# Kernel tuning notes

Hardware: AMD Instinct MI355X
Metric: run time of the kernel (lower is better)

Reference implementation:

```python
import jax, jax.numpy as jnp
import numpy as np

N_NODES = 50000
IN_F = 512
OUT_F = 512
N_EDGES = 1600000
DROP_P = 0.5
NEG_SLOPE = 0.01  # torch LeakyReLU default


def leaky_relu(x):
    return jnp.where(x >= 0, x, NEG_SLOPE * x)


def setup_inputs() -> dict:
    key = jax.random.key(0)
    k1, k2, k3, k4, k5, k6 = jax.random.split(key, 6)
    x = jax.random.normal(k1, (N_NODES, IN_F), dtype=jnp.float32)
    W = jax.random.normal(k2, (OUT_F, IN_F), dtype=jnp.float32) * (1.0 / np.sqrt(IN_F))
    # inverted dropout mask: bernoulli(keep)/keep, keep = 1 - p
    keep = 1.0 - DROP_P
    drop_mask = (jax.random.uniform(k3, (N_NODES, IN_F)) < keep).astype(jnp.float32) / keep
    adj_vals = jax.random.uniform(k4, (N_EDGES,), dtype=jnp.float32)
    adj_rows = jax.random.randint(k5, (N_EDGES,), 0, N_NODES, dtype=jnp.int32)
    adj_cols = jax.random.randint(k6, (N_EDGES,), 0, N_NODES, dtype=jnp.int32)
    return {"x": x, "W": W, "drop_mask": drop_mask, "adj_vals": adj_vals,
            "adj_rows": adj_rows, "adj_cols": adj_cols}


def reference(x, W, drop_mask, adj_vals, adj_rows, adj_cols):
    # support = Linear(dropout(x)); Linear weight is [out, in] (torch convention)
    support = jnp.einsum('ni,oi->no', x * drop_mask, W)  # [N, out]
    h = leaky_relu(support)
    # sparse adj @ h: out[r] += v * h[c]
    msgs = adj_vals[:, None] * h[adj_cols]               # [E, out]
    agg = jax.ops.segment_sum(msgs, adj_rows, num_segments=N_NODES)
    return leaky_relu(agg)
```

## Files before the change

kernel.cpp:

```cpp
#include <hip/hip_runtime.h>

#define NROWS 50000
#define NFEAT 512
#define NEDGE 1600000
#define SLOPE 0.01f

typedef unsigned short u16;
typedef __attribute__((ext_vector_type(8))) short short8;
typedef __attribute__((ext_vector_type(4))) float f32x4;
typedef __attribute__((ext_vector_type(4))) int i32x4;
typedef __attribute__((ext_vector_type(2))) unsigned uintx2;
typedef __attribute__((ext_vector_type(8))) unsigned short u16x8;

__device__ __forceinline__ u16 f2bf(float f) {
  unsigned u = __float_as_uint(f);
  u += 0x7fffu + ((u >> 16) & 1u);
  return (u16)(u >> 16);
}
__device__ __forceinline__ float lrelu(float v) { return v >= 0.f ? v : SLOPE * v; }

__device__ __forceinline__ void gload_lds16(const u16* g, u16* l) {
  __builtin_amdgcn_global_load_lds((const __attribute__((address_space(1))) void*)g,
                                   (__attribute__((address_space(3))) void*)l, 16, 0, 0);
}

__global__ void prep_kernel(const float* __restrict__ x, const float* __restrict__ m,
                            u16* __restrict__ xd, const float* __restrict__ w,
                            u16* __restrict__ wb, const int* __restrict__ rows,
                            int* __restrict__ counts) {
  const int stride = gridDim.x * blockDim.x;
  const int tid0 = blockIdx.x * blockDim.x + threadIdx.x;
  for (int i = tid0; i < (NROWS * NFEAT) / 8; i += stride) {
    size_t b = (size_t)i * 2;
    f32x4 a0 = __builtin_nontemporal_load(&((const f32x4*)x)[b]);
    f32x4 a1 = __builtin_nontemporal_load(&((const f32x4*)x)[b + 1]);
    f32x4 m0 = __builtin_nontemporal_load(&((const f32x4*)m)[b]);
    f32x4 m1 = __builtin_nontemporal_load(&((const f32x4*)m)[b + 1]);
    u16x8 o;
    o[0] = f2bf(a0[0] * m0[0]); o[1] = f2bf(a0[1] * m0[1]);
    o[2] = f2bf(a0[2] * m0[2]); o[3] = f2bf(a0[3] * m0[3]);
    o[4] = f2bf(a1[0] * m1[0]); o[5] = f2bf(a1[1] * m1[1]);
    o[6] = f2bf(a1[2] * m1[2]); o[7] = f2bf(a1[3] * m1[3]);
    *(u16x8*)(xd + (size_t)i * 8) = o;
  }
  for (int i = tid0; i < (NFEAT * NFEAT) / 8; i += stride) {
    size_t b = (size_t)i * 2;
    f32x4 a0 = __builtin_nontemporal_load(&((const f32x4*)w)[b]);
    f32x4 a1 = __builtin_nontemporal_load(&((const f32x4*)w)[b + 1]);
    u16x8 o;
    o[0] = f2bf(a0[0]); o[1] = f2bf(a0[1]); o[2] = f2bf(a0[2]); o[3] = f2bf(a0[3]);
    o[4] = f2bf(a1[0]); o[5] = f2bf(a1[1]); o[6] = f2bf(a1[2]); o[7] = f2bf(a1[3]);
    *(u16x8*)(wb + (size_t)i * 8) = o;
  }
  for (int i = tid0; i < NEDGE / 4; i += stride) {
    i32x4 r4 = __builtin_nontemporal_load(&((const i32x4*)rows)[i]);
    atomicAdd(&counts[r4[0]], 1);
    atomicAdd(&counts[r4[1]], 1);
    atomicAdd(&counts[r4[2]], 1);
    atomicAdd(&counts[r4[3]], 1);
  }
}

__global__ void scan_kernel(const int* __restrict__ counts, int* __restrict__ offs) {
  __shared__ int wpre[17];
  const int t = threadIdx.x;
  const int lane = t & 63, w = t >> 6;
  const int beg = t * 64;
  i32x4 c4[16];
  int s = 0;
  if (beg < NROWS) {
#pragma unroll
    for (int g = 0; g < 16; ++g) {
      int idx = beg + g * 4;
      if (idx < NROWS) {
        c4[g] = ((const i32x4*)counts)[idx >> 2];
        s += c4[g][0] + c4[g][1] + c4[g][2] + c4[g][3];
      }
    }
  }
  int inc = s;
#pragma unroll
  for (int d = 1; d < 64; d <<= 1) {
    int u = __shfl_up(inc, d);
    if (lane >= d) inc += u;
  }
  if (lane == 63) wpre[w + 1] = inc;
  __syncthreads();
  if (t == 0) {
    wpre[0] = 0;
    for (int i = 1; i <= 16; ++i) wpre[i] += wpre[i - 1];
    offs[NROWS] = wpre[16];
  }
  __syncthreads();
  int run = wpre[w] + inc - s;
  if (beg < NROWS) {
#pragma unroll
    for (int g = 0; g < 16; ++g) {
      int idx = beg + g * 4;
      if (idx < NROWS) {
        i32x4 o;
        o[0] = run; run += c4[g][0];
        o[1] = run; run += c4[g][1];
        o[2] = run; run += c4[g][2];
        o[3] = run; run += c4[g][3];
        ((i32x4*)offs)[idx >> 2] = o;
      }
    }
  }
}

__global__ void scatter_kernel(const float* __restrict__ vals, const int* __restrict__ rows,
                               const int* __restrict__ cols, const int* __restrict__ offs,
                               int* __restrict__ cursor, unsigned* __restrict__ svc) {
  int e0 = (blockIdx.x * blockDim.x + threadIdx.x) * 4;
  if (e0 >= NEDGE) return;
  i32x4 r4 = __builtin_nontemporal_load((const i32x4*)(rows + e0));
  i32x4 c4 = __builtin_nontemporal_load((const i32x4*)(cols + e0));
  f32x4 v4 = __builtin_nontemporal_load((const f32x4*)(vals + e0));
#pragma unroll
  for (int j = 0; j < 4; ++j) {
    int p = offs[r4[j]] + atomicAdd(&cursor[r4[j]], 1);
    svc[p] = ((unsigned)c4[j] << 16) | (unsigned)f2bf(v4[j]);
  }
}

__global__ __launch_bounds__(256) void gemm_kernel(const u16* __restrict__ xd,
                                                   const u16* __restrict__ wb,
                                                   unsigned char* __restrict__ hq,
                                                   float* __restrict__ scaleg) {
  __shared__ __align__(16) u16 lAB[2 * 128 * 64];
  __shared__ float wmax[2][128];
  __shared__ float rinv[128];
  u16* lA = lAB;
  u16* lB = lAB + 128 * 64;
  const int tid = threadIdx.x;
  const int lane = tid & 63;
  const int wid = tid >> 6;
  const int wm = wid >> 1, wn = wid & 1;
  const int bx0 = blockIdx.x;
  const int xcd = bx0 & 7, idx = bx0 >> 3;
  const int wg = (xcd < 4 ? xcd * 196 : 784 + (xcd - 4) * 195) + idx;
  const int tm = wg >> 2;
  const int tn = wg & 3;
  const long rowBase = (long)tm * 128;

  f32x4 acc[4][4] = {};

  const int sl8 = lane >> 3;
  const int scol = ((lane & 7) ^ sl8) * 8;
  const int rsel = lane & 15, kgrp = (lane >> 4) * 8;

  for (int k0 = 0; k0 < 512; k0 += 64) {
    __syncthreads();
#pragma unroll
    for (int c = 0; c < 4; ++c) {
      int rbase = wid * 32 + c * 8;
      long gr = rowBase + rbase + sl8;
      if (gr > NROWS - 1) gr = NROWS - 1;
      gload_lds16(xd + gr * 512 + k0 + scol, lA + rbase * 64);
      gload_lds16(wb + ((long)tn * 128 + rbase + sl8) * 512 + k0 + scol, lB + rbase * 64);
    }
    __syncthreads();
    short8 a[4][2], b[4][2];
#pragma unroll
    for (int m = 0; m < 4; ++m) {
      int ar = wm * 64 + m * 16 + rsel;
      const u16* base = lA + ar * 64;
      int sw = (ar & 7) << 3;
      a[m][0] = *(const short8*)(base + (kgrp ^ sw));
      a[m][1] = *(const short8*)(base + ((32 + kgrp) ^ sw));
    }
#pragma unroll
    for (int n = 0; n < 4; ++n) {
      int br = wn * 64 + n * 16 + rsel;
      const u16* base = lB + br * 64;
      int sw = (br & 7) << 3;
      b[n][0] = *(const short8*)(base + (kgrp ^ sw));
      b[n][1] = *(const short8*)(base + ((32 + kgrp) ^ sw));
    }
#pragma unroll
    for (int kk = 0; kk < 2; ++kk)
#pragma unroll
      for (int m = 0; m < 4; ++m)
#pragma unroll
        for (int n = 0; n < 4; ++n)
          acc[m][n] = __builtin_amdgcn_mfma_f32_16x16x32_bf16(a[m][kk], b[n][kk], acc[m][n], 0, 0, 0);
  }

  const int crow = (lane >> 4) * 4;
  const int ccol = lane & 15;

  float pm[4][4];
#pragma unroll
  for (int m = 0; m < 4; ++m)
#pragma unroll
    for (int r2 = 0; r2 < 4; ++r2) {
      float mx = 0.f;
#pragma unroll
      for (int n = 0; n < 4; ++n) mx = fmaxf(mx, fabsf(lrelu(acc[m][n][r2])));
      pm[m][r2] = mx;
    }
#pragma unroll
  for (int d = 1; d < 16; d <<= 1)
#pragma unroll
    for (int m = 0; m < 4; ++m)
#pragma unroll
      for (int r2 = 0; r2 < 4; ++r2) pm[m][r2] = fmaxf(pm[m][r2], __shfl_xor(pm[m][r2], d));
  if ((lane & 15) == 0) {
#pragma unroll
    for (int m = 0; m < 4; ++m)
#pragma unroll
      for (int r2 = 0; r2 < 4; ++r2) wmax[wn][wm * 64 + m * 16 + crow + r2] = pm[m][r2];
  }
  __syncthreads();
  if (tid < 128) {
    float rm = fmaxf(wmax[0][tid], wmax[1][tid]);
    float s = rm > 0.f ? rm * (1.f / 127.f) : 1.f;
    rinv[tid] = rm > 0.f ? 127.f / rm : 0.f;
    long gr = rowBase + tid;
    if (gr < NROWS) scaleg[gr * 4 + tn] = s;
  }
  __syncthreads();

  unsigned char* lT = (unsigned char*)lAB;
#pragma unroll
  for (int m = 0; m < 4; ++m) {
    int row0 = wm * 64 + m * 16 + crow;
    float ri0 = rinv[row0], ri1 = rinv[row0 + 1], ri2 = rinv[row0 + 2], ri3 = rinv[row0 + 3];
#pragma unroll
    for (int n = 0; n < 4; ++n) {
      int col = wn * 64 + n * 16 + ccol;
      float q0 = rintf(lrelu(acc[m][n][0]) * ri0);
      float q1 = rintf(lrelu(acc[m][n][1]) * ri1);
      float q2 = rintf(lrelu(acc[m][n][2]) * ri2);
      float q3 = rintf(lrelu(acc[m][n][3]) * ri3);
      int i0 = min(127, max(-127, (int)q0));
      int i1 = min(127, max(-127, (int)q1));
      int i2 = min(127, max(-127, (int)q2));
      int i3 = min(127, max(-127, (int)q3));
      unsigned pk = (i0 & 0xff) | ((i1 & 0xff) << 8) | ((i2 & 0xff) << 16) | ((i3 & 0xff) << 24);
#pragma unroll
      for (int r2 = 0; r2 < 4; ++r2) {
        int row = row0 + r2;
        lT[row * 128 + (col ^ ((row & 7) << 4))] = (unsigned char)(pk >> (8 * r2));
      }
    }
  }
  __syncthreads();
  {
    const int row = tid >> 1, seg = tid & 1;
    long gr = rowBase + row;
    if (gr < NROWS) {
      unsigned char* dst = hq + gr * 512 + tn * 128;
#pragma unroll
      for (int j = 0; j < 4; ++j) {
        int s = seg * 4 + j;
        i32x4 vv = *(const i32x4*)(lT + row * 128 + ((s ^ (row & 7)) << 4));
        *(i32x4*)(dst + s * 16) = vv;
      }
    }
  }
}

__global__ __launch_bounds__(256) void aggregate_kernel(const unsigned char* __restrict__ hq,
                                                        const float* __restrict__ scaleg,
                                                        const unsigned* __restrict__ svc,
                                                        const int* __restrict__ offs,
                                                        float* __restrict__ out) {
  const int lane = threadIdx.x & 63;
  const int wid = threadIdx.x >> 6;
  const int r = blockIdx.x * 4 + wid;
  if (r >= NROWS) return;
  const int beg = offs[r], end = offs[r + 1];
  const int grp = lane >> 4;
  float a[8] = {};
  const unsigned char* hp = hq + lane * 8;
  unsigned cb[8], nb[8];
  const int ng = (end - beg) >> 3;
  if (ng > 0) {
#pragma unroll
    for (int k = 0; k < 8; ++k) cb[k] = __builtin_nontemporal_load(&svc[beg + k]);
  }
  for (int g = 0; g < ng; ++g) {
    if (g + 1 < ng) {
#pragma unroll
      for (int k = 0; k < 8; ++k) nb[k] = __builtin_nontemporal_load(&svc[beg + (g + 1) * 8 + k]);
    }
#pragma unroll
    for (int k = 0; k < 8; ++k) {
      float v = __uint_as_float(cb[k] << 16);
      size_t c = (size_t)(cb[k] >> 16);
      float vs = v * scaleg[c * 4 + grp];
      uintx2 q = *(const uintx2*)(hp + c * 512);
      a[0] += vs * (float)(signed char)(q[0]);
      a[1] += vs * (float)(signed char)(q[0] >> 8);
      a[2] += vs * (float)(signed char)(q[0] >> 16);
      a[3] += vs * (float)(signed char)(q[0] >> 24);
      a[4] += vs * (float)(signed char)(q[1]);
      a[5] += vs * (float)(signed char)(q[1] >> 8);
      a[6] += vs * (float)(signed char)(q[1] >> 16);
      a[7] += vs * (float)(signed char)(q[1] >> 24);
    }
    if (g + 1 < ng) {
#pragma unroll
      for (int k = 0; k < 8; ++k) cb[k] = nb[k];
    }
  }
  for (int e = beg + ng * 8; e < end; ++e) {
    unsigned q2 = __builtin_nontemporal_load(&svc[e]);
    float v = __uint_as_float(q2 << 16);
    size_t c = (size_t)(q2 >> 16);
    float vs = v * scaleg[c * 4 + grp];
    uintx2 q = *(const uintx2*)(hp + c * 512);
    a[0] += vs * (float)(signed char)(q[0]);
    a[1] += vs * (float)(signed char)(q[0] >> 8);
    a[2] += vs * (float)(signed char)(q[0] >> 16);
    a[3] += vs * (float)(signed char)(q[0] >> 24);
    a[4] += vs * (float)(signed char)(q[1]);
    a[5] += vs * (float)(signed char)(q[1] >> 8);
    a[6] += vs * (float)(signed char)(q[1] >> 16);
    a[7] += vs * (float)(signed char)(q[1] >> 24);
  }
  float* op = out + (size_t)r * NFEAT + lane * 8;
  f32x4 o0, o1;
  o0[0] = lrelu(a[0]); o0[1] = lrelu(a[1]); o0[2] = lrelu(a[2]); o0[3] = lrelu(a[3]);
  o1[0] = lrelu(a[4]); o1[1] = lrelu(a[5]); o1[2] = lrelu(a[6]); o1[3] = lrelu(a[7]);
  __builtin_nontemporal_store(o0, (f32x4*)op);
  __builtin_nontemporal_store(o1, (f32x4*)(op + 4));
}

extern "C" void kernel_launch(void* const* d_in, const int* in_sizes, int n_in,
                              void* d_out, int out_size, void* d_ws, size_t ws_size,
                              hipStream_t stream) {
  const float* x = (const float*)d_in[0];
  const float* W = (const float*)d_in[1];
  const float* mask = (const float*)d_in[2];
  const float* vals = (const float*)d_in[3];
  const int* rows = (const int*)d_in[4];
  const int* cols = (const int*)d_in[5];
  float* out = (float*)d_out;
  char* ws = (char*)d_ws;

  const size_t o_xd = 0;
  const size_t o_hq = o_xd + 51200000;
  const size_t o_wb = o_hq + 25600000;
  const size_t o_scale = o_wb + 524288;
  const size_t o_counts = o_scale + 800000;
  const size_t o_cursor = o_counts + 200000;
  const size_t o_offs = o_cursor + 200000;
  const size_t o_svc = o_offs + 200064;

  u16* xd = (u16*)(ws + o_xd);
  unsigned char* hq = (unsigned char*)(ws + o_hq);
  u16* wb = (u16*)(ws + o_wb);
  float* scaleg = (float*)(ws + o_scale);
  int* counts = (int*)(ws + o_counts);
  int* cursor = (int*)(ws + o_cursor);
  int* offs = (int*)(ws + o_offs);
  unsigned* svc = (unsigned*)(ws + o_svc);

  hipMemsetAsync(counts, 0, 400000, stream);

  prep_kernel<<<2048, 256, 0, stream>>>(x, mask, xd, W, wb, rows, counts);
  scan_kernel<<<1, 1024, 0, stream>>>(counts, offs);
  scatter_kernel<<<1563, 256, 0, stream>>>(vals, rows, cols, offs, cursor, svc);
  gemm_kernel<<<391 * 4, 256, 0, stream>>>(xd, wb, hq, scaleg);
  aggregate_kernel<<<12500, 256, 0, stream>>>(hq, scaleg, svc, offs, out);
}
```

Baseline: 404.9 us.

## Read GEMM B operand straight from global and split aggregate edges across half-waves

The GEMM no longer stages the weight tile in LDS; each lane loads its B fragments directly from global memory, which halves LDS use and removes the B LDS traffic at the cost of uncoalesced, cache-dependent global reads. The aggregate kernel splits each wave into two 32-lane halves that handle alternating edges with 16-byte gathers per lane. The halves are combined with a cross-half shuffle before the output store, which now uses regular rather than nontemporal stores. This targets more memory-level parallelism in the gather and fewer, wider loads.

```diff
diff --git a/kernel.cpp b/kernel.cpp
--- a/kernel.cpp
+++ b/kernel.cpp
@@ -9,7 +9,6 @@
 typedef __attribute__((ext_vector_type(8))) short short8;
 typedef __attribute__((ext_vector_type(4))) float f32x4;
 typedef __attribute__((ext_vector_type(4))) int i32x4;
-typedef __attribute__((ext_vector_type(2))) unsigned uintx2;
 typedef __attribute__((ext_vector_type(8))) unsigned short u16x8;
 
 __device__ __forceinline__ u16 f2bf(float f) {
@@ -128,11 +127,9 @@
                                                    const u16* __restrict__ wb,
                                                    unsigned char* __restrict__ hq,
                                                    float* __restrict__ scaleg) {
-  __shared__ __align__(16) u16 lAB[2 * 128 * 64];
+  __shared__ __align__(16) u16 lA[128 * 64];
   __shared__ float wmax[2][128];
   __shared__ float rinv[128];
-  u16* lA = lAB;
-  u16* lB = lAB + 128 * 64;
   const int tid = threadIdx.x;
   const int lane = tid & 63;
   const int wid = tid >> 6;
@@ -149,6 +146,7 @@
   const int sl8 = lane >> 3;
   const int scol = ((lane & 7) ^ sl8) * 8;
   const int rsel = lane & 15, kgrp = (lane >> 4) * 8;
+  const u16* bbase = wb + ((long)(tn * 128 + wn * 64 + rsel)) * 512 + kgrp;
 
   for (int k0 = 0; k0 < 512; k0 += 64) {
     __syncthreads();
@@ -158,10 +156,16 @@
       long gr = rowBase + rbase + sl8;
       if (gr > NROWS - 1) gr = NROWS - 1;
       gload_lds16(xd + gr * 512 + k0 + scol, lA + rbase * 64);
-      gload_lds16(wb + ((long)tn * 128 + rbase + sl8) * 512 + k0 + scol, lB + rbase * 64);
+    }
+    short8 b[4][2];
+#pragma unroll
+    for (int n = 0; n < 4; ++n) {
+#pragma unroll
+      for (int kk = 0; kk < 2; ++kk)
+        b[n][kk] = *(const short8*)(bbase + (long)n * 16 * 512 + k0 + kk * 32);
     }
     __syncthreads();
-    short8 a[4][2], b[4][2];
+    short8 a[4][2];
 #pragma unroll
     for (int m = 0; m < 4; ++m) {
       int ar = wm * 64 + m * 16 + rsel;
@@ -171,14 +175,6 @@
       a[m][1] = *(const short8*)(base + ((32 + kgrp) ^ sw));
     }
 #pragma unroll
-    for (int n = 0; n < 4; ++n) {
-      int br = wn * 64 + n * 16 + rsel;
-      const u16* base = lB + br * 64;
-      int sw = (br & 7) << 3;
-      b[n][0] = *(const short8*)(base + (kgrp ^ sw));
-      b[n][1] = *(const short8*)(base + ((32 + kgrp) ^ sw));
-    }
-#pragma unroll
     for (int kk = 0; kk < 2; ++kk)
 #pragma unroll
       for (int m = 0; m < 4; ++m)
@@ -222,7 +218,7 @@
   }
   __syncthreads();
 
-  unsigned char* lT = (unsigned char*)lAB;
+  unsigned char* lT = (unsigned char*)lA;
 #pragma unroll
   for (int m = 0; m < 4; ++m) {
     int row0 = wm * 64 + m * 16 + crow;
@@ -272,61 +268,87 @@
   const int r = blockIdx.x * 4 + wid;
   if (r >= NROWS) return;
   const int beg = offs[r], end = offs[r + 1];
-  const int grp = lane >> 4;
-  float a[8] = {};
-  const unsigned char* hp = hq + lane * 8;
-  unsigned cb[8], nb[8];
-  const int ng = (end - beg) >> 3;
+  const int half = lane >> 5, sub = lane & 31;
+  const int grp = sub >> 3;
+  float a[16] = {};
+  const unsigned char* hp = hq + sub * 16;
+  unsigned cb[4], nb[4];
+  const int n = end - beg;
+  const int ng = n >> 3;
   if (ng > 0) {
 #pragma unroll
-    for (int k = 0; k < 8; ++k) cb[k] = __builtin_nontemporal_load(&svc[beg + k]);
+    for (int k = 0; k < 4; ++k) cb[k] = svc[beg + 2 * k + half];
   }
   for (int g = 0; g < ng; ++g) {
     if (g + 1 < ng) {
 #pragma unroll
-      for (int k = 0; k < 8; ++k) nb[k] = __builtin_nontemporal_load(&svc[beg + (g + 1) * 8 + k]);
-    }
-#pragma unroll
-    for (int k = 0; k < 8; ++k) {
+      for (int k = 0; k < 4; ++k) nb[k] = svc[beg + (g + 1) * 8 + 2 * k + half];
+    }
+#pragma unroll
+    for (int k = 0; k < 4; ++k) {
       float v = __uint_as_float(cb[k] << 16);
       size_t c = (size_t)(cb[k] >> 16);
       float vs = v * scaleg[c * 4 + grp];
-      uintx2 q = *(const uintx2*)(hp + c * 512);
-      a[0] += vs * (float)(signed char)(q[0]);
-      a[1] += vs * (float)(signed char)(q[0] >> 8);
-      a[2] += vs * (float)(signed char)(q[0] >> 16);
-      a[3] += vs * (float)(signed char)(q[0] >> 24);
-      a[4] += vs * (float)(signed char)(q[1]);
-      a[5] += vs * (float)(signed char)(q[1] >> 8);
-      a[6] += vs * (float)(signed char)(q[1] >> 16);
-      a[7] += vs * (float)(signed char)(q[1] >> 24);
+      i32x4 q = *(const i32x4*)(hp + c * 512);
+#pragma unroll
+      for (int j = 0; j < 4; ++j) {
+        unsigned qq = (unsigned)q[j];
+        a[4 * j + 0] += vs * (float)(signed char)(qq);
+        a[4 * j + 1] += vs * (float)(signed char)(qq >> 8);
+        a[4 * j + 2] += vs * (float)(signed char)(qq >> 16);
+        a[4 * j + 3] += vs * (float)(signed char)(qq >> 24);
+      }
     }
     if (g + 1 < ng) {
 #pragma unroll
-      for (int k = 0; k < 8; ++k) cb[k] = nb[k];
-    }
-  }
-  for (int e = beg + ng * 8; e < end; ++e) {
-    unsigned q2 = __builtin_nontemporal_load(&svc[e]);
-    float v = __uint_as_float(q2 << 16);
-    size_t c = (size_t)(q2 >> 16);
+      for (int k = 0; k < 4; ++k) cb[k] = nb[k];
+    }
+  }
+  int e = beg + ng * 8;
+  for (; e + 1 < end; e += 2) {
+    unsigned u = svc[e + half];
+    float v = __uint_as_float(u << 16);
+    size_t c = (size_t)(u >> 16);
     float vs = v * scaleg[c * 4 + grp];
-    uintx2 q = *(const uintx2*)(hp + c * 512);
-    a[0] += vs * (float)(signed char)(q[0]);
-    a[1] += vs * (float)(signed char)(q[0] >> 8);
-    a[2] += vs * (float)(signed char)(q[0] >> 16);
-    a[3] += vs * (float)(signed char)(q[0] >> 24);
-    a[4] += vs * (float)(signed char)(q[1]);
-    a[5] += vs * (float)(signed char)(q[1] >> 8);
-    a[6] += vs * (float)(signed char)(q[1] >> 16);
-    a[7] += vs * (float)(signed char)(q[1] >> 24);
-  }
-  float* op = out + (size_t)r * NFEAT + lane * 8;
-  f32x4 o0, o1;
-  o0[0] = lrelu(a[0]); o0[1] = lrelu(a[1]); o0[2] = lrelu(a[2]); o0[3] = lrelu(a[3]);
-  o1[0] = lrelu(a[4]); o1[1] = lrelu(a[5]); o1[2] = lrelu(a[6]); o1[3] = lrelu(a[7]);
-  __builtin_nontemporal_store(o0, (f32x4*)op);
-  __builtin_nontemporal_store(o1, (f32x4*)(op + 4));
+    i32x4 q = *(const i32x4*)(hp + c * 512);
+#pragma unroll
+    for (int j = 0; j < 4; ++j) {
+      unsigned qq = (unsigned)q[j];
+      a[4 * j + 0] += vs * (float)(signed char)(qq);
+      a[4 * j + 1] += vs * (float)(signed char)(qq >> 8);
+      a[4 * j + 2] += vs * (float)(signed char)(qq >> 16);
+      a[4 * j + 3] += vs * (float)(signed char)(qq >> 24);
+    }
+  }
+  if (e < end) {
+    unsigned u = svc[e];
+    float v = __uint_as_float(u << 16);
+    size_t c = (size_t)(u >> 16);
+    float vs = half ? 0.f : v * scaleg[c * 4 + grp];
+    i32x4 q = *(const i32x4*)(hp + c * 512);
+#pragma unroll
+    for (int j = 0; j < 4; ++j) {
+      unsigned qq = (unsigned)q[j];
+      a[4 * j + 0] += vs * (float)(signed char)(qq);
+      a[4 * j + 1] += vs * (float)(signed char)(qq >> 8);
+      a[4 * j + 2] += vs * (float)(signed char)(qq >> 16);
+      a[4 * j + 3] += vs * (float)(signed char)(qq >> 24);
+    }
+  }
+#pragma unroll
+  for (int j = 0; j < 16; ++j) a[j] += __shfl_xor(a[j], 32);
+  if (half == 0) {
+    float* op = out + (size_t)r * NFEAT + sub * 16;
+#pragma unroll
+    for (int j = 0; j < 4; ++j) {
+      f32x4 o;
+      o[0] = lrelu(a[4 * j + 0]);
+      o[1] = lrelu(a[4 * j + 1]);
+      o[2] = lrelu(a[4 * j + 2]);
+      o[3] = lrelu(a[4 * j + 3]);
+      *(f32x4*)(op + 4 * j) = o;
+    }
+  }
 }
 
 extern "C" void kernel_launch(void* const* d_in, const int* in_sizes, int n_in,
```

Result: no change. 403.6 us (-0.3%).

## Split aggregation across 8 feature slices and load GEMM B operand directly from global

Applied to the files above, without the earlier changes.

The aggregate kernel now launches 8x more blocks. Each wave handles a 64-column slice of a row, and each lane gathers one int8 feature per edge instead of eight, which adds parallelism and memory-level concurrency. The cost is re-reading the edge list and scales eight times per row, with byte-sized gathers. Separately, the GEMM stops staging W tiles in LDS and has each wave load its B fragments straight from global into registers, halving LDS use but losing the shared reuse of B across waves.

```diff
diff --git a/kernel.cpp b/kernel.cpp
--- a/kernel.cpp
+++ b/kernel.cpp
@@ -9,7 +9,6 @@
 typedef __attribute__((ext_vector_type(8))) short short8;
 typedef __attribute__((ext_vector_type(4))) float f32x4;
 typedef __attribute__((ext_vector_type(4))) int i32x4;
-typedef __attribute__((ext_vector_type(2))) unsigned uintx2;
 typedef __attribute__((ext_vector_type(8))) unsigned short u16x8;
 
 __device__ __forceinline__ u16 f2bf(float f) {
@@ -128,11 +127,9 @@
                                                    const u16* __restrict__ wb,
                                                    unsigned char* __restrict__ hq,
                                                    float* __restrict__ scaleg) {
-  __shared__ __align__(16) u16 lAB[2 * 128 * 64];
+  __shared__ __align__(16) u16 lA[128 * 64];
   __shared__ float wmax[2][128];
   __shared__ float rinv[128];
-  u16* lA = lAB;
-  u16* lB = lAB + 128 * 64;
   const int tid = threadIdx.x;
   const int lane = tid & 63;
   const int wid = tid >> 6;
@@ -149,6 +146,7 @@
   const int sl8 = lane >> 3;
   const int scol = ((lane & 7) ^ sl8) * 8;
   const int rsel = lane & 15, kgrp = (lane >> 4) * 8;
+  const u16* bbase = wb + ((long)(tn * 128 + wn * 64 + rsel)) * 512 + kgrp;
 
   for (int k0 = 0; k0 < 512; k0 += 64) {
     __syncthreads();
@@ -158,10 +156,16 @@
       long gr = rowBase + rbase + sl8;
       if (gr > NROWS - 1) gr = NROWS - 1;
       gload_lds16(xd + gr * 512 + k0 + scol, lA + rbase * 64);
-      gload_lds16(wb + ((long)tn * 128 + rbase + sl8) * 512 + k0 + scol, lB + rbase * 64);
+    }
+    short8 b[4][2];
+#pragma unroll
+    for (int n = 0; n < 4; ++n) {
+#pragma unroll
+      for (int kk = 0; kk < 2; ++kk)
+        b[n][kk] = *(const short8*)(bbase + (long)n * 16 * 512 + k0 + kk * 32);
     }
     __syncthreads();
-    short8 a[4][2], b[4][2];
+    short8 a[4][2];
 #pragma unroll
     for (int m = 0; m < 4; ++m) {
       int ar = wm * 64 + m * 16 + rsel;
@@ -171,14 +175,6 @@
       a[m][1] = *(const short8*)(base + ((32 + kgrp) ^ sw));
     }
 #pragma unroll
-    for (int n = 0; n < 4; ++n) {
-      int br = wn * 64 + n * 16 + rsel;
-      const u16* base = lB + br * 64;
-      int sw = (br & 7) << 3;
-      b[n][0] = *(const short8*)(base + (kgrp ^ sw));
-      b[n][1] = *(const short8*)(base + ((32 + kgrp) ^ sw));
-    }
-#pragma unroll
     for (int kk = 0; kk < 2; ++kk)
 #pragma unroll
       for (int m = 0; m < 4; ++m)
@@ -222,7 +218,7 @@
   }
   __syncthreads();
 
-  unsigned char* lT = (unsigned char*)lAB;
+  unsigned char* lT = (unsigned char*)lA;
 #pragma unroll
   for (int m = 0; m < 4; ++m) {
     int row0 = wm * 64 + m * 16 + crow;
@@ -262,71 +258,53 @@
   }
 }
 
-__global__ __launch_bounds__(256) void aggregate_kernel(const unsigned char* __restrict__ hq,
+__global__ __launch_bounds__(256) void aggregate_kernel(const signed char* __restrict__ hq,
                                                         const float* __restrict__ scaleg,
                                                         const unsigned* __restrict__ svc,
                                                         const int* __restrict__ offs,
                                                         float* __restrict__ out) {
   const int lane = threadIdx.x & 63;
-  const int wid = threadIdx.x >> 6;
-  const int r = blockIdx.x * 4 + wid;
+  const int wv = threadIdx.x >> 6;
+  const int slice = blockIdx.x & 7;
+  const int r = (blockIdx.x >> 3) * 4 + wv;
   if (r >= NROWS) return;
+  const int grp = slice >> 1;
   const int beg = offs[r], end = offs[r + 1];
-  const int grp = lane >> 4;
-  float a[8] = {};
-  const unsigned char* hp = hq + lane * 8;
-  unsigned cb[8], nb[8];
-  const int ng = (end - beg) >> 3;
+  const signed char* hp = hq + slice * 64 + lane;
+  const float* sg = scaleg + grp;
+  float acc = 0.f;
+  const int n = end - beg;
+  const int ng = n >> 3;
+  unsigned cu[8], nu[8];
   if (ng > 0) {
 #pragma unroll
-    for (int k = 0; k < 8; ++k) cb[k] = __builtin_nontemporal_load(&svc[beg + k]);
+    for (int k = 0; k < 8; ++k) cu[k] = svc[beg + k];
   }
   for (int g = 0; g < ng; ++g) {
     if (g + 1 < ng) {
 #pragma unroll
-      for (int k = 0; k < 8; ++k) nb[k] = __builtin_nontemporal_load(&svc[beg + (g + 1) * 8 + k]);
-    }
+      for (int k = 0; k < 8; ++k) nu[k] = svc[beg + (g + 1) * 8 + k];
+    }
+    float vs[8], qv[8];
 #pragma unroll
     for (int k = 0; k < 8; ++k) {
-      float v = __uint_as_float(cb[k] << 16);
-      size_t c = (size_t)(cb[k] >> 16);
-      float vs = v * scaleg[c * 4 + grp];
-      uintx2 q = *(const uintx2*)(hp + c * 512);
-      a[0] += vs * (float)(signed char)(q[0]);
-      a[1] += vs * (float)(signed char)(q[0] >> 8);
-      a[2] += vs * (float)(signed char)(q[0] >> 16);
-      a[3] += vs * (float)(signed char)(q[0] >> 24);
-      a[4] += vs * (float)(signed char)(q[1]);
-      a[5] += vs * (float)(signed char)(q[1] >> 8);
-      a[6] += vs * (float)(signed char)(q[1] >> 16);
-      a[7] += vs * (float)(signed char)(q[1] >> 24);
-    }
+      unsigned c = cu[k] >> 16;
+      vs[k] = __uint_as_float(cu[k] << 16) * sg[c * 4];
+      qv[k] = (float)hp[(size_t)c * 512];
+    }
+#pragma unroll
+    for (int k = 0; k < 8; ++k) acc += vs[k] * qv[k];
     if (g + 1 < ng) {
 #pragma unroll
-      for (int k = 0; k < 8; ++k) cb[k] = nb[k];
+      for (int k = 0; k < 8; ++k) cu[k] = nu[k];
     }
   }
   for (int e = beg + ng * 8; e < end; ++e) {
-    unsigned q2 = __builtin_nontemporal_load(&svc[e]);
-    float v = __uint_as_float(q2 << 16);
-    size_t c = (size_t)(q2 >> 16);
-    float vs = v * scaleg[c * 4 + grp];
-    uintx2 q = *(const uintx2*)(hp + c * 512);
-    a[0] += vs * (float)(signed char)(q[0]);
-    a[1] += vs * (float)(signed char)(q[0] >> 8);
-    a[2] += vs * (float)(signed char)(q[0] >> 16);
-    a[3] += vs * (float)(signed char)(q[0] >> 24);
-    a[4] += vs * (float)(signed char)(q[1]);
-    a[5] += vs * (float)(signed char)(q[1] >> 8);
-    a[6] += vs * (float)(signed char)(q[1] >> 16);
-    a[7] += vs * (float)(signed char)(q[1] >> 24);
-  }
-  float* op = out + (size_t)r * NFEAT + lane * 8;
-  f32x4 o0, o1;
-  o0[0] = lrelu(a[0]); o0[1] = lrelu(a[1]); o0[2] = lrelu(a[2]); o0[3] = lrelu(a[3]);
-  o1[0] = lrelu(a[4]); o1[1] = lrelu(a[5]); o1[2] = lrelu(a[6]); o1[3] = lrelu(a[7]);
-  __builtin_nontemporal_store(o0, (f32x4*)op);
-  __builtin_nontemporal_store(o1, (f32x4*)(op + 4));
+    unsigned u = svc[e];
+    unsigned c = u >> 16;
+    acc += __uint_as_float(u << 16) * sg[c * 4] * (float)hp[(size_t)c * 512];
+  }
+  __builtin_nontemporal_store(lrelu(acc), out + (size_t)r * NFEAT + slice * 64 + lane);
 }
 
 extern "C" void kernel_launch(void* const* d_in, const int* in_sizes, int n_in,
@@ -365,5 +343,5 @@
   scan_kernel<<<1, 1024, 0, stream>>>(counts, offs);
   scatter_kernel<<<1563, 256, 0, stream>>>(vals, rows, cols, offs, cursor, svc);
   gemm_kernel<<<391 * 4, 256, 0, stream>>>(xd, wb, hq, scaleg);
-  aggregate_kernel<<<12500, 256, 0, stream>>>(hq, scaleg, svc, offs, out);
-}
+  aggregate_kernel<<<12500 * 8, 256, 0, stream>>>((const signed char*)hq, scaleg, svc, offs, out);
+}
```

New measurement: 609.9 us. 50.6% more time.
